# Kernel optimization log

Measured on AMD Instinct MI355X. Metric: run time of the kernel, lower is better.

The kernel has to match this reference:

```python
import jax, jax.numpy as jnp
import numpy as np
from jax import lax

KSIZE, STRIDE, RATE, SOFTMAX_SCALE = 3, 1, 2, 10.0


def extract_patches(x, k, stride):
    # x: [B,C,H,W] -> [B,C,k,k,oh,ow]; torch-style zero 'same' padding
    B, C, H, W = x.shape
    oh, ow = -(-H // stride), -(-W // stride)
    ph = max(0, (oh - 1) * stride + k - H)
    pw = max(0, (ow - 1) * stride + k - W)
    x = jnp.pad(x, ((0, 0), (0, 0), (ph // 2, ph - ph // 2), (pw // 2, pw - pw // 2)))
    cols = [x[:, :, i:i + (oh - 1) * stride + 1:stride, j:j + (ow - 1) * stride + 1:stride]
            for i in range(k) for j in range(k)]
    return jnp.stack(cols, axis=2).reshape(B, C, k, k, oh, ow)


def setup_inputs():
    key = jax.random.key(0)
    kf, kb = jax.random.split(key)
    f = jax.random.normal(kf, (2, 128, 128, 128), dtype=jnp.float32)
    b = jax.random.normal(kb, (2, 128, 128, 128), dtype=jnp.float32)
    mask = jnp.zeros((2, 1, 512, 512), dtype=jnp.float32)
    mask = mask.at[:, :, 128:384, 128:384].set(1.0)  # central hole: bg patches unavailable
    return {"f": f, "b": b, "mask": mask}


def reference(f, b, mask):
    B, C, H, W = b.shape
    kernel = 2 * RATE
    # raw background patches used for reconstruction (stride = rate*stride)
    raw = extract_patches(b, kernel, RATE * STRIDE)            # [B,C,4,4,Hb,Wb]
    Hb, Wb = raw.shape[-2:]
    L = Hb * Wb
    raw_w = raw.transpose(0, 4, 5, 1, 2, 3).reshape(B, L, C, kernel, kernel)
    # nearest 1/rate downsample (integer rate -> strided slice)
    fs = f[:, :, ::RATE, ::RATE]
    bs = b[:, :, ::RATE, ::RATE]
    Hf, Wf = fs.shape[-2:]
    # matching patches from downsampled background, L2-normalized per patch
    wp = extract_patches(bs, KSIZE, STRIDE)                    # [B,C,3,3,Hb,Wb]
    w = wp.transpose(0, 4, 5, 1, 2, 3).reshape(B, L, C, KSIZE, KSIZE)
    norm = jnp.sqrt(jnp.sum(w * w, axis=(2, 3, 4), keepdims=True))
    w_normed = w / jnp.maximum(norm, 1e-4)
    # mask -> per-patch validity (original uses batch element 0 only)
    ms = mask[:, :, ::4 * RATE, ::4 * RATE]                    # [B,1,Hb,Wb]
    mp = extract_patches(ms, KSIZE, STRIDE)[0]                 # [1,3,3,Hb,Wb]
    mm = (jnp.mean(mp, axis=(0, 1, 2)).reshape(-1) == 0.0).astype(f.dtype)
    mm = mm.reshape(1, L, 1, 1)
    # similarity scores: per-image conv2d of fg with bg patches == patch einsum
    fp = extract_patches(fs, KSIZE, STRIDE)                    # [B,C,3,3,Hf,Wf]
    yi = jnp.einsum('bcpqhw,blcpq->blhw', fp, w_normed)        # [B,L,Hf,Wf]
    yi = yi * mm
    yi = jax.nn.softmax(yi * SOFTMAX_SCALE, axis=1)
    yi = yi * mm
    # argmax offsets relative to reference coordinates (int_bs == int_fs here)
    off = jnp.argmax(yi, axis=1)                               # [B,Hf,Wf]
    h_ref = jnp.arange(Hf)[None, :, None]
    w_ref = jnp.arange(Wf)[None, None, :]
    offsets = jnp.stack([off // Wf - h_ref, off % Wf - w_ref], axis=1)  # [B,2,Hf,Wf]
    # reconstruction: conv_transpose2d(yi, raw_wi, stride=rate, padding=1) / 4
    w_ct = jnp.flip(raw_w.transpose(0, 2, 1, 3, 4), axis=(-2, -1))      # [B,C,L,4,4]
    pad = kernel - 1 - 1  # transpose-conv padding=1 -> conv pad k-1-1
    def ct(a, wk):
        return lax.conv_general_dilated(a[None], wk, (1, 1),
                                        ((pad, pad), (pad, pad)),
                                        lhs_dilation=(RATE, RATE),
                                        dimension_numbers=('NCHW', 'OIHW', 'NCHW'))[0]
    y = jax.vmap(ct)(yi, w_ct) / 4.0                           # [B,C,H,W]
    return y, offsets
```

## Files before the change

### kernel.cpp

```cpp
#include <hip/hip_runtime.h>
#include <hip/hip_bf16.h>
#include <cstdint>

#define B_  2
#define C_  128
#define HH  128
#define WW  128
#define L_  4096
#define K1  1152
#define M2  2048
#define NPAD 3072
#define NCAND 16
#define MARGIN 0.15f
#define PCUT 5e-4f
#define MAXC 512

typedef __attribute__((ext_vector_type(8))) short bf16x8s;
typedef __attribute__((ext_vector_type(4))) float f32x4;
typedef __attribute__((ext_vector_type(2))) float f32x2;
using bf16 = __hip_bfloat16;

__device__ inline float bf16bits2f(unsigned short s) {
  uint32_t u = ((uint32_t)s) << 16;
  return __builtin_bit_cast(float, u);
}
__device__ inline unsigned short f2bf16bits(float x) {
  uint32_t u = __builtin_bit_cast(uint32_t, x);
  u += 0x7fffu + ((u >> 16) & 1u);
  return (unsigned short)(u >> 16);
}

__device__ inline uint8_t fp8_encode(float v) {
  uint32_t s = (__builtin_bit_cast(uint32_t, v) >> 24) & 0x80u;
  float av = fabsf(v);
  uint32_t byte;
  if (av >= 0.015625f) {
    uint32_t bits = __builtin_bit_cast(uint32_t, av);
    uint32_t mant = bits & 0x7fffffu;
    uint32_t E = bits >> 23;
    uint32_t m3 = (mant + 0x7ffffu + ((mant >> 20) & 1u)) >> 20;
    if (m3 == 8u) { m3 = 0u; E++; }
    int e8 = (int)E - 120;
    if (e8 > 15) { e8 = 15; m3 = 6; }
    byte = ((uint32_t)e8 << 3) | m3;
  } else {
    byte = (uint32_t)(av * 512.f + 0.5f);
  }
  return (uint8_t)(s | byte);
}

#if __has_builtin(__builtin_amdgcn_cvt_pk_f32_fp8)
#define FP8PK(d, hi) __builtin_amdgcn_cvt_pk_f32_fp8((d), (hi))
#else
__device__ inline f32x2 FP8PK(uint32_t d, bool hi) {
  uint32_t b0 = hi ? ((d >> 16) & 0xffu) : (d & 0xffu);
  uint32_t b1 = hi ? (d >> 24) : ((d >> 8) & 0xffu);
  f32x2 r;
  r.x = __builtin_bit_cast(float, ((b0 & 0x80u) << 24) | ((b0 & 0x7fu) << 20)) * 0x1p120f;
  r.y = __builtin_bit_cast(float, ((b1 & 0x80u) << 24) | ((b1 & 0x7fu) << 20)) * 0x1p120f;
  return r;
}
#endif

__device__ inline void gload_lds16(const void* g, void* l) {
  auto gp = reinterpret_cast<const __attribute__((address_space(1))) uint32_t*>(
      reinterpret_cast<uintptr_t>(g));
  auto lp = reinterpret_cast<__attribute__((address_space(3))) uint32_t*>(
      reinterpret_cast<uintptr_t>(l));
  __builtin_amdgcn_global_load_lds(gp, lp, 16, 0, 0);
}

__global__ void compute_mm_k(const float* __restrict__ mask, float* __restrict__ mm) {
  int l = blockIdx.x * 256 + threadIdx.x;
  if (l >= L_) return;
  int i = l >> 6, j = l & 63;
  float s = 0.f;
  for (int p = -1; p <= 1; ++p)
    for (int q = -1; q <= 1; ++q) {
      int y = i + p, x = j + q;
      if ((unsigned)y < 64u && (unsigned)x < 64u)
        s += mask[(size_t)(8 * y) * 512 + 8 * x];
    }
  mm[l] = (s == 0.f) ? 1.f : 0.f;
}

__global__ __launch_bounds__(256) void compact_k(const float* __restrict__ mm,
                                                 int* __restrict__ vlist,
                                                 int* __restrict__ vmap,
                                                 int* __restrict__ meta) {
  __shared__ int wpart[4];
  int t = threadIdx.x;
  int lane = t & 63, wid = t >> 6;
  int loc[16];
  int cnt = 0;
#pragma unroll
  for (int s = 0; s < 16; ++s) {
    int l = t * 16 + s;
    loc[s] = cnt;
    cnt += (mm[l] != 0.f) ? 1 : 0;
  }
  int pre = cnt;
#pragma unroll
  for (int o = 1; o < 64; o <<= 1) {
    int u = __shfl_up(pre, o);
    if (lane >= o) pre += u;
  }
  if (lane == 63) wpart[wid] = pre;
  int excl = pre - cnt;
  __syncthreads();
  int base = 0;
  for (int w = 0; w < wid; ++w) base += wpart[w];
  int mybase = base + excl;
#pragma unroll
  for (int s = 0; s < 16; ++s) {
    int l = t * 16 + s;
    if (mm[l] != 0.f) {
      int pos = mybase + loc[s];
      vlist[pos] = l;
      vmap[l] = pos;
    }
  }
  if (t == 0) {
    int total = wpart[0] + wpart[1] + wpart[2] + wpart[3];
    meta[0] = total;
    meta[1] = L_ - total;
  }
}

__global__ __launch_bounds__(256) void prep_u_k(const float* __restrict__ bsrc,
                                                const float* __restrict__ mm,
                                                const int* __restrict__ vmap,
                                                bf16* __restrict__ Ucomp,
                                                float* __restrict__ U32) {
  __shared__ float red[4];
  int l = blockIdx.x;
  int bi = blockIdx.y;
  if (mm[l] == 0.f) return;
  int pos = vmap[l];
  int i = l >> 6, j = l & 63;
  int t = threadIdx.x;
  float vals[5];
  float ss = 0.f;
#pragma unroll
  for (int s = 0; s < 5; ++s) {
    int k = t + s * 256;
    float v = 0.f;
    if (k < K1) {
      int c = k / 9, r = k - c * 9;
      int p = r / 3, q = r - p * 3;
      int y = i + p - 1, x = j + q - 1;
      if ((unsigned)y < 64u && (unsigned)x < 64u)
        v = bsrc[(((size_t)bi * C_ + c) * HH + 2 * y) * WW + 2 * x];
    }
    vals[s] = v;
    ss += v * v;
  }
#pragma unroll
  for (int o = 32; o; o >>= 1) ss += __shfl_xor(ss, o);
  if ((t & 63) == 0) red[t >> 6] = ss;
  __syncthreads();
  float tot = red[0] + red[1] + red[2] + red[3];
  float den = fmaxf(sqrtf(tot), 1e-4f);
  float inv = 1.f / den;
  size_t cbase = ((size_t)bi * NPAD + pos) * K1;
  size_t obase = ((size_t)bi * L_ + l) * K1;
#pragma unroll
  for (int s = 0; s < 5; ++s) {
    int k = t + s * 256;
    if (k < K1) {
      float u = vals[s] * inv;
      Ucomp[cbase + k] = __float2bfloat16(u);
      U32[obase + k] = u;
    }
  }
}

__global__ __launch_bounds__(256) void prep_fp_k(const float* __restrict__ f,
                                                 bf16* __restrict__ FP,
                                                 float* __restrict__ FP32) {
  int idx = blockIdx.x * 256 + threadIdx.x;
  int bi = blockIdx.y;
  if (idx >= L_ * K1) return;
  int hw = idx / K1, k = idx - hw * K1;
  int h = hw >> 6, w = hw & 63;
  int c = k / 9, r = k - c * 9;
  int p = r / 3, q = r - p * 3;
  int y = h + p - 1, x = w + q - 1;
  float v = 0.f;
  if ((unsigned)y < 64u && (unsigned)x < 64u)
    v = f[(((size_t)bi * C_ + c) * HH + 2 * y) * WW + 2 * x];
  size_t o = (size_t)bi * L_ * K1 + idx;
  FP[o] = __float2bfloat16(v);
  FP32[o] = v;
}

__global__ void prep_bmatT_k(const float* __restrict__ bsrc, uint8_t* __restrict__ BmT8) {
  int idx = blockIdx.x * 256 + threadIdx.x;
  int bi = blockIdx.y;
  if (idx >= M2 * L_) return;
  int l = idx >> 11, m = idx & 2047;
  int c = m >> 4, p = (m >> 2) & 3, q = m & 3;
  int i = l >> 6, j = l & 63;
  int y = 2 * i + p - 1, x = 2 * j + q - 1;
  float v = 0.f;
  if ((unsigned)y < 128u && (unsigned)x < 128u)
    v = bsrc[(((size_t)bi * C_ + c) * HH + y) * WW + x];
  BmT8[(size_t)bi * M2 * L_ + idx] = fp8_encode(v);
}

__global__ __launch_bounds__(256) void gemm_bt(const bf16* __restrict__ A,
                                               const bf16* __restrict__ Bbase,
                                               bf16* __restrict__ C,
                                               int N, int K) {
  __shared__ __align__(16) bf16 sA[2][128][32];
  __shared__ __align__(16) bf16 sB[2][128][32];
  const int tid = threadIdx.x;
  const int lane = tid & 63;
  const int wid = tid >> 6;
  const int bm = blockIdx.x * 128;
  const int bn = blockIdx.y * 128;
  const bf16* B = Bbase + (size_t)(bm >> 12) * NPAD * K1;
  const int wm = (wid >> 1) * 64;
  const int wn = (wid & 1) * 64;
  const int lrow = lane & 15;
  const int lko = (lane >> 4) * 8;

  f32x4 acc[4][4];
#pragma unroll
  for (int i = 0; i < 4; ++i)
#pragma unroll
    for (int j = 0; j < 4; ++j) acc[i][j] = (f32x4){0.f, 0.f, 0.f, 0.f};

  const int nt = K >> 5;
  const int s0 = tid, s1 = tid + 256;
  const int ar0 = s0 >> 2, ac0 = (s0 & 3) * 8;
  const int ar1 = s1 >> 2, ac1 = (s1 & 3) * 8;

  auto STAGE = [&](int bufi, int t) {
    const int k0 = t * 32;
    gload_lds16(A + (size_t)(bm + ar0) * K + k0 + ac0, &sA[bufi][ar0][ac0]);
    gload_lds16(A + (size_t)(bm + ar1) * K + k0 + ac1, &sA[bufi][ar1][ac1]);
    gload_lds16(B + (size_t)(bn + ar0) * K + k0 + ac0, &sB[bufi][ar0][ac0]);
    gload_lds16(B + (size_t)(bn + ar1) * K + k0 + ac1, &sB[bufi][ar1][ac1]);
  };

  STAGE(0, 0);
  __syncthreads();
  int buf = 0;
  for (int t = 0; t < nt; ++t) {
    if (t + 1 < nt) STAGE(buf ^ 1, t + 1);
    bf16x8s af[4], bfr[4];
#pragma unroll
    for (int fm = 0; fm < 4; ++fm)
      af[fm] = *(const bf16x8s*)&sA[buf][wm + fm * 16 + lrow][lko];
#pragma unroll
    for (int fn = 0; fn < 4; ++fn)
      bfr[fn] = *(const bf16x8s*)&sB[buf][wn + fn * 16 + lrow][lko];
#pragma unroll
    for (int fm = 0; fm < 4; ++fm)
#pragma unroll
      for (int fn = 0; fn < 4; ++fn)
        acc[fm][fn] = __builtin_amdgcn_mfma_f32_16x16x32_bf16(af[fm], bfr[fn], acc[fm][fn], 0, 0, 0);
    __syncthreads();
    buf ^= 1;
  }

  const int crow = (lane >> 4) * 4;
  const int ccol = lane & 15;
#pragma unroll
  for (int fm = 0; fm < 4; ++fm)
#pragma unroll
    for (int fn = 0; fn < 4; ++fn) {
      int r0 = bm + wm + fm * 16 + crow;
      int c0 = bn + wn + fn * 16 + ccol;
#pragma unroll
      for (int r = 0; r < 4; ++r)
        C[(size_t)(r0 + r) * N + c0] = __float2bfloat16(acc[fm][fn][r]);
    }
}

__global__ __launch_bounds__(256) void softmax_spmv_k(const bf16* __restrict__ Sb,
                                                      const int* __restrict__ vlist,
                                                      const int* __restrict__ meta,
                                                      const uint8_t* __restrict__ BmT8b,
                                                      unsigned short* __restrict__ Ztb,
                                                      int* __restrict__ candb,
                                                      int* __restrict__ candcntb) {
  __shared__ float rmax[4];
  __shared__ float rsum[4];
  __shared__ int scnt, mcnt;
  __shared__ int slist[MAXC];
  __shared__ float splist[MAXC];
  __shared__ int mlist[NCAND];
  const int row = blockIdx.x;
  const int bi = blockIdx.y;
  const int t = threadIdx.x;
  const int vcnt = meta[0];
  const int nmask = meta[1];
  const uint8_t* BmT8 = BmT8b + (size_t)bi * M2 * L_;
  if (t == 0) { scnt = 0; mcnt = 0; }
  const bool has = (t < NPAD / 16);
  const int c0 = t * 16;
  float xs[16];
#pragma unroll
  for (int s = 0; s < 16; ++s) xs[s] = -1e30f;
  if (has) {
    const bf16* srow = Sb + ((size_t)bi * L_ + row) * NPAD;
    bf16x8s sv0 = *(const bf16x8s*)&srow[c0];
    bf16x8s sv1 = *(const bf16x8s*)&srow[c0 + 8];
#pragma unroll
    for (int s = 0; s < 8; ++s) {
      xs[s] = bf16bits2f((unsigned short)sv0[s]);
      xs[s + 8] = bf16bits2f((unsigned short)sv1[s]);
    }
  }
  float vmax = -1e30f;
#pragma unroll
  for (int s = 0; s < 16; ++s)
    if (has && c0 + s < vcnt) vmax = fmaxf(vmax, xs[s]);
#pragma unroll
  for (int o = 32; o; o >>= 1) vmax = fmaxf(vmax, __shfl_xor(vmax, o));
  if ((t & 63) == 0) rmax[t >> 6] = vmax;
  __syncthreads();
  vmax = fmaxf(fmaxf(rmax[0], rmax[1]), fmaxf(rmax[2], rmax[3]));
  float gmax = (nmask > 0) ? fmaxf(vmax, 0.f) : vmax;
  float zs = 0.f;
#pragma unroll
  for (int s = 0; s < 16; ++s)
    if (has && c0 + s < vcnt) zs += __expf(10.f * (xs[s] - gmax));
#pragma unroll
  for (int o = 32; o; o >>= 1) zs += __shfl_xor(zs, o);
  if ((t & 63) == 0) rsum[t >> 6] = zs;
  __syncthreads();
  zs = rsum[0] + rsum[1] + rsum[2] + rsum[3] + (float)nmask * __expf(-10.f * gmax);
  float invZ = 1.f / zs;
  float cutx = gmax + __logf(PCUT * zs) * 0.1f;
  if (has) {
#pragma unroll
    for (int s = 0; s < 16; ++s) {
      int c = c0 + s;
      if (c < vcnt) {
        if (xs[s] >= cutx) {
          int pos = atomicAdd(&scnt, 1);
          if (pos < MAXC) {
            slist[pos] = vlist[c];
            splist[pos] = __expf(10.f * (xs[s] - gmax)) * invZ;
          }
        }
        if (xs[s] >= vmax - MARGIN) {
          int pos = atomicAdd(&mcnt, 1);
          if (pos < NCAND) mlist[pos] = vlist[c];
        }
      }
    }
  }
  __syncthreads();
  int nc = min(scnt, MAXC);
  float acc[8] = {0.f, 0.f, 0.f, 0.f, 0.f, 0.f, 0.f, 0.f};
#pragma unroll 4
  for (int ci = 0; ci < nc; ++ci) {
    int l = slist[ci];
    float p = splist[ci];
    const uint32_t* bp = (const uint32_t*)(BmT8 + (size_t)l * M2) + t * 2;
    uint32_t d0 = bp[0], d1 = bp[1];
    f32x2 w0 = FP8PK(d0, false);
    f32x2 w1 = FP8PK(d0, true);
    f32x2 w2 = FP8PK(d1, false);
    f32x2 w3 = FP8PK(d1, true);
    acc[0] += p * w0.x; acc[1] += p * w0.y;
    acc[2] += p * w1.x; acc[3] += p * w1.y;
    acc[4] += p * w2.x; acc[5] += p * w2.y;
    acc[6] += p * w3.x; acc[7] += p * w3.y;
  }
  bf16x8s zv;
#pragma unroll
  for (int j = 0; j < 8; ++j) zv[j] = (short)f2bf16bits(acc[j]);
  *(bf16x8s*)&Ztb[((size_t)bi * L_ + row) * M2 + t * 8] = zv;
  if (t == 0) candcntb[bi * L_ + row] = min(mcnt, NCAND);
  if (t < NCAND && t < mcnt) candb[(bi * L_ + row) * NCAND + t] = mlist[t];
}

__global__ __launch_bounds__(256) void transpose_k(const unsigned short* __restrict__ inb,
                                                   unsigned short* __restrict__ outb) {
  __shared__ ushort2 tile[32][33];
  int bi = blockIdx.z;
  const unsigned short* in = inb + (size_t)bi * L_ * M2;
  unsigned short* out = outb + (size_t)bi * M2 * L_;
  int bm2 = blockIdx.x * 32;
  int bh = blockIdx.y * 32;
  int tx = threadIdx.x & 31;
  int ty = threadIdx.x >> 5;
  const ushort2* in2 = (const ushort2*)in;
#pragma unroll
  for (int r = 0; r < 32; r += 8)
    tile[ty + r][tx] = in2[(size_t)(bh + ty + r) * (M2 / 2) + bm2 + tx];
  __syncthreads();
#pragma unroll
  for (int r = 0; r < 32; r += 8) {
    ushort2 v = tile[tx][ty + r];
    int mp = bm2 + ty + r;
    out[(size_t)(2 * mp) * L_ + bh + tx] = v.x;
    out[(size_t)(2 * mp + 1) * L_ + bh + tx] = v.y;
  }
}

__global__ __launch_bounds__(256) void rescore_k(const float* __restrict__ FP32b,
                                                 const float* __restrict__ U32b,
                                                 const int* __restrict__ candb,
                                                 const int* __restrict__ candcntb,
                                                 float* __restrict__ offout) {
  __shared__ float red[4];
  const int row = blockIdx.x;
  const int bi = blockIdx.y;
  const int t = threadIdx.x;
  const int h = row >> 6, w = row & 63;
  const float* FP32 = FP32b + (size_t)bi * L_ * K1;
  const float* U32 = U32b + (size_t)bi * L_ * K1;
  const int* cand = candb + (size_t)(bi * L_ + row) * NCAND;
  int cnt = candcntb[bi * L_ + row];
  int bestl;
  if (cnt <= 1) {
    bestl = cand[0];
  } else {
    float fv[5];
#pragma unroll
    for (int s = 0; s < 5; ++s) {
      int k = t + s * 256;
      fv[s] = (k < K1) ? FP32[(size_t)row * K1 + k] : 0.f;
    }
    float bestv = -1e30f;
    bestl = 0x7fffffff;
    for (int ci = 0; ci < cnt; ++ci) {
      int l = cand[ci];
      const float* urow = U32 + (size_t)l * K1;
      float dot = 0.f;
#pragma unroll
      for (int s = 0; s < 5; ++s) {
        int k = t + s * 256;
        if (k < K1) dot += fv[s] * urow[k];
      }
#pragma unroll
      for (int o = 32; o; o >>= 1) dot += __shfl_xor(dot, o);
      if ((t & 63) == 0) red[t >> 6] = dot;
      __syncthreads();
      dot = red[0] + red[1] + red[2] + red[3];
      if (dot > bestv || (dot == bestv && l < bestl)) { bestv = dot; bestl = l; }
      __syncthreads();
    }
  }
  if (t == 0) {
    int istar = bestl >> 6, jstar = bestl & 63;
    offout[(size_t)bi * 8192 + row] = (float)(istar - h);
    offout[(size_t)bi * 8192 + L_ + row] = (float)(jstar - w);
  }
}

__global__ void gather_k(const unsigned short* __restrict__ Z2b, float* __restrict__ yout) {
  int u = blockIdx.x, c = blockIdx.y, bi = blockIdx.z;
  int t = threadIdx.x;
  const unsigned short* Z2 = Z2b + (size_t)bi * M2 * L_;
  int h0 = (u + 1) >> 1, p0 = (u + 1) & 1;
  int h1 = h0 - 1, p1 = p0 + 2;
  float a0 = 0.f, a1 = 0.f;
#pragma unroll
  for (int e = 0; e < 2; ++e) {
    int h = e ? h1 : h0;
    int p = e ? p1 : p0;
    if ((unsigned)h < 64u) {
      const unsigned short* zb = Z2 + (size_t)(c * 16 + p * 4) * L_ + h * 64;
      a0 += bf16bits2f(zb[1 * L_ + t]);
      if (t >= 1) a0 += bf16bits2f(zb[3 * L_ + (t - 1)]);
      if (t < 63) a1 += bf16bits2f(zb[0 * L_ + (t + 1)]);
      a1 += bf16bits2f(zb[2 * L_ + t]);
    }
  }
  size_t ybase = (((size_t)bi * C_ + c) * HH + u) * WW;
  yout[ybase + 2 * t] = a0 * 0.25f;
  yout[ybase + 2 * t + 1] = a1 * 0.25f;
}

extern "C" void kernel_launch(void* const* d_in, const int* in_sizes, int n_in,
                              void* d_out, int out_size, void* d_ws, size_t ws_size,
                              hipStream_t stream) {
  const float* f = (const float*)d_in[0];
  const float* b = (const float*)d_in[1];
  const float* mask = (const float*)d_in[2];
  float* out = (float*)d_out;
  char* ws = (char*)d_ws;

  size_t off = 0;
  float* mm = (float*)(ws + off);          off += 16384;
  int* vlist = (int*)(ws + off);           off += 16384;
  int* vmap = (int*)(ws + off);            off += 16384;
  int* meta = (int*)(ws + off);            off += 16384;
  int* cand = (int*)(ws + off);            off += (size_t)B_ * L_ * NCAND * 4;
  int* candcnt = (int*)(ws + off);         off += 65536;
  bf16* Ucomp = (bf16*)(ws + off);         off += (size_t)B_ * NPAD * K1 * 2;
  bf16* FP = (bf16*)(ws + off);            off += (size_t)B_ * L_ * K1 * 2;
  float* U32 = (float*)(ws + off);         off += (size_t)B_ * L_ * K1 * 4;
  float* FP32 = (float*)(ws + off);        off += (size_t)B_ * L_ * K1 * 4;
  uint8_t* BmT8 = (uint8_t*)(ws + off);    off += (size_t)B_ * M2 * L_;
  bf16* S = (bf16*)(ws + off);             off += (size_t)B_ * L_ * NPAD * 2;
  unsigned short* Zt = (unsigned short*)(ws + off); off += (size_t)B_ * M2 * L_ * 2;
  unsigned short* Z2 = (unsigned short*)(ws + off); off += (size_t)B_ * M2 * L_ * 2;
  float* yout = out;
  float* offout = out + (size_t)B_ * C_ * HH * WW;

  compute_mm_k<<<16, 256, 0, stream>>>(mask, mm);
  compact_k<<<1, 256, 0, stream>>>(mm, vlist, vmap, meta);
  prep_u_k<<<dim3(L_, B_), 256, 0, stream>>>(b, mm, vmap, Ucomp, U32);
  prep_fp_k<<<dim3((L_ * K1 + 255) / 256, B_), 256, 0, stream>>>(f, FP, FP32);
  prep_bmatT_k<<<dim3((M2 * L_ + 255) / 256, B_), 256, 0, stream>>>(b, BmT8);
  gemm_bt<<<dim3(B_ * L_ / 128, NPAD / 128), 256, 0, stream>>>(FP, Ucomp, S, NPAD, K1);
  softmax_spmv_k<<<dim3(L_, B_), 256, 0, stream>>>(S, vlist, meta, BmT8, Zt, cand, candcnt);
  rescore_k<<<dim3(L_, B_), 256, 0, stream>>>(FP32, U32, cand, candcnt, offout);
  transpose_k<<<dim3(M2 / 64, L_ / 32, B_), 256, 0, stream>>>(Zt, Z2);
  gather_k<<<dim3(128, 128, B_), 64, 0, stream>>>(Z2, yout);
}
```

Measured before the change: 256.9 us.

## Enlarge GEMM tiles to 256x256 with triple-buffered LDS pipeline

The similarity GEMM moves from 128x128 tiles with 256 threads and double buffering to 256x256 tiles with 512 threads, 8x4 MFMA fragments per wave, and a three-slot LDS ring. Loads are issued two stages ahead, with manual vmcnt waits and s_barrier in place of __syncthreads. MFMA sections are wrapped in s_setprio. The aim is more data reuse per LDS byte and better hiding of global-load latency, at the cost of more registers and fewer blocks (32x12 grid), which could reduce occupancy and load balance.

```diff
diff --git a/kernel.cpp b/kernel.cpp
--- a/kernel.cpp
+++ b/kernel.cpp
@@ -14,6 +14,11 @@
 #define MARGIN 0.15f
 #define PCUT 5e-4f
 #define MAXC 512
+
+#define BMG 256
+#define BNG 256
+#define BKG 32
+#define NBUF 3
 
 typedef __attribute__((ext_vector_type(8))) short bf16x8s;
 typedef __attribute__((ext_vector_type(4))) float f32x4;
@@ -208,67 +213,84 @@
   BmT8[(size_t)bi * M2 * L_ + idx] = fp8_encode(v);
 }
 
-__global__ __launch_bounds__(256) void gemm_bt(const bf16* __restrict__ A,
-                                               const bf16* __restrict__ Bbase,
-                                               bf16* __restrict__ C,
-                                               int N, int K) {
-  __shared__ __align__(16) bf16 sA[2][128][32];
-  __shared__ __align__(16) bf16 sB[2][128][32];
+__global__ __launch_bounds__(512, 2) void gemm_bt(const bf16* __restrict__ A,
+                                                  const bf16* __restrict__ Bbase,
+                                                  bf16* __restrict__ C,
+                                                  int N, int K) {
+  extern __shared__ char smem[];
+  bf16 (*sA)[BMG][BKG] = (bf16(*)[BMG][BKG])smem;
+  bf16 (*sB)[BNG][BKG] = (bf16(*)[BNG][BKG])(smem + (size_t)NBUF * BMG * BKG * 2);
   const int tid = threadIdx.x;
   const int lane = tid & 63;
   const int wid = tid >> 6;
-  const int bm = blockIdx.x * 128;
-  const int bn = blockIdx.y * 128;
+  const int bm = blockIdx.x * BMG;
+  const int bn = blockIdx.y * BNG;
   const bf16* B = Bbase + (size_t)(bm >> 12) * NPAD * K1;
-  const int wm = (wid >> 1) * 64;
-  const int wn = (wid & 1) * 64;
+  const int wm = (wid >> 2) * 128;
+  const int wn = (wid & 3) * 64;
   const int lrow = lane & 15;
   const int lko = (lane >> 4) * 8;
 
-  f32x4 acc[4][4];
-#pragma unroll
-  for (int i = 0; i < 4; ++i)
+  f32x4 acc[8][4];
+#pragma unroll
+  for (int i = 0; i < 8; ++i)
 #pragma unroll
     for (int j = 0; j < 4; ++j) acc[i][j] = (f32x4){0.f, 0.f, 0.f, 0.f};
 
   const int nt = K >> 5;
-  const int s0 = tid, s1 = tid + 256;
-  const int ar0 = s0 >> 2, ac0 = (s0 & 3) * 8;
-  const int ar1 = s1 >> 2, ac1 = (s1 & 3) * 8;
-
-  auto STAGE = [&](int bufi, int t) {
-    const int k0 = t * 32;
-    gload_lds16(A + (size_t)(bm + ar0) * K + k0 + ac0, &sA[bufi][ar0][ac0]);
-    gload_lds16(A + (size_t)(bm + ar1) * K + k0 + ac1, &sA[bufi][ar1][ac1]);
-    gload_lds16(B + (size_t)(bn + ar0) * K + k0 + ac0, &sB[bufi][ar0][ac0]);
-    gload_lds16(B + (size_t)(bn + ar1) * K + k0 + ac1, &sB[bufi][ar1][ac1]);
+  const int srow = tid >> 2;
+  const int scol = (tid & 3) * 8;
+
+  auto STAGE = [&](int slot, int t) {
+    const int k0 = t * BKG;
+    gload_lds16(A + (size_t)(bm + srow) * K + k0 + scol,        &sA[slot][srow][scol]);
+    gload_lds16(A + (size_t)(bm + 128 + srow) * K + k0 + scol,  &sA[slot][128 + srow][scol]);
+    gload_lds16(B + (size_t)(bn + srow) * K + k0 + scol,        &sB[slot][srow][scol]);
+    gload_lds16(B + (size_t)(bn + 128 + srow) * K + k0 + scol,  &sB[slot][128 + srow][scol]);
   };
 
   STAGE(0, 0);
-  __syncthreads();
-  int buf = 0;
+  STAGE(1, 1);
+  asm volatile("s_waitcnt vmcnt(4)" ::: "memory");
+  asm volatile("s_barrier" ::: "memory");
+
+  int slot = 0;
   for (int t = 0; t < nt; ++t) {
-    if (t + 1 < nt) STAGE(buf ^ 1, t + 1);
-    bf16x8s af[4], bfr[4];
-#pragma unroll
-    for (int fm = 0; fm < 4; ++fm)
-      af[fm] = *(const bf16x8s*)&sA[buf][wm + fm * 16 + lrow][lko];
+    int s2 = slot + 2; if (s2 >= NBUF) s2 -= NBUF;
+    if (t + 2 < nt) STAGE(s2, t + 2);
+
+    bf16x8s bfr[4];
 #pragma unroll
     for (int fn = 0; fn < 4; ++fn)
-      bfr[fn] = *(const bf16x8s*)&sB[buf][wn + fn * 16 + lrow][lko];
-#pragma unroll
-    for (int fm = 0; fm < 4; ++fm)
-#pragma unroll
-      for (int fn = 0; fn < 4; ++fn)
-        acc[fm][fn] = __builtin_amdgcn_mfma_f32_16x16x32_bf16(af[fm], bfr[fn], acc[fm][fn], 0, 0, 0);
-    __syncthreads();
-    buf ^= 1;
+      bfr[fn] = *(const bf16x8s*)&sB[slot][wn + fn * 16 + lrow][lko];
+#pragma unroll
+    for (int half = 0; half < 2; ++half) {
+      bf16x8s af[4];
+#pragma unroll
+      for (int fm = 0; fm < 4; ++fm)
+        af[fm] = *(const bf16x8s*)&sA[slot][wm + (half * 4 + fm) * 16 + lrow][lko];
+      __builtin_amdgcn_s_setprio(1);
+#pragma unroll
+      for (int fm = 0; fm < 4; ++fm)
+#pragma unroll
+        for (int fn = 0; fn < 4; ++fn)
+          acc[half * 4 + fm][fn] =
+              __builtin_amdgcn_mfma_f32_16x16x32_bf16(af[fm], bfr[fn], acc[half * 4 + fm][fn], 0, 0, 0);
+      __builtin_amdgcn_s_setprio(0);
+    }
+
+    if (t + 1 < nt) {
+      if (t + 2 < nt) asm volatile("s_waitcnt vmcnt(4)" ::: "memory");
+      else            asm volatile("s_waitcnt vmcnt(0)" ::: "memory");
+      asm volatile("s_barrier" ::: "memory");
+    }
+    slot = (slot + 1 == NBUF) ? 0 : slot + 1;
   }
 
   const int crow = (lane >> 4) * 4;
   const int ccol = lane & 15;
 #pragma unroll
-  for (int fm = 0; fm < 4; ++fm)
+  for (int fm = 0; fm < 8; ++fm)
 #pragma unroll
     for (int fn = 0; fn < 4; ++fn) {
       int r0 = bm + wm + fm * 16 + crow;
@@ -511,7 +533,8 @@
   prep_u_k<<<dim3(L_, B_), 256, 0, stream>>>(b, mm, vmap, Ucomp, U32);
   prep_fp_k<<<dim3((L_ * K1 + 255) / 256, B_), 256, 0, stream>>>(f, FP, FP32);
   prep_bmatT_k<<<dim3((M2 * L_ + 255) / 256, B_), 256, 0, stream>>>(b, BmT8);
-  gemm_bt<<<dim3(B_ * L_ / 128, NPAD / 128), 256, 0, stream>>>(FP, Ucomp, S, NPAD, K1);
+  gemm_bt<<<dim3(B_ * L_ / BMG, NPAD / BNG), 512,
+            (size_t)NBUF * (BMG + BNG) * BKG * 2, stream>>>(FP, Ucomp, S, NPAD, K1);
   softmax_spmv_k<<<dim3(L_, B_), 256, 0, stream>>>(S, vlist, meta, BmT8, Zt, cand, candcnt);
   rescore_k<<<dim3(L_, B_), 256, 0, stream>>>(FP32, U32, cand, candcnt, offout);
   transpose_k<<<dim3(M2 / 64, L_ / 32, B_), 256, 0, stream>>>(Zt, Z2);
```

New measurement: 262.7 us. +2.3%, slower.

## Triple-buffer GEMM LDS staging with split-phase MFMA and priority hints

Applied to the files above, without the earlier changes.

Moves the bf16 GEMM from a double-buffered to a triple-buffered LDS pipeline that prefetches two K-tiles ahead. Each iteration is split into two MFMA phases, with the A and B loads for a future tile interleaved between them. Explicit vmcnt waits, raw s_barriers and s_setprio are used to keep the matrix units busy while global-to-LDS copies are in flight. LDS use grows by half, which may reduce occupancy, and the extra barriers plus the hand-written waitcnt logic add synchronisation and correctness risk.

```diff
diff --git a/kernel.cpp b/kernel.cpp
--- a/kernel.cpp
+++ b/kernel.cpp
@@ -212,8 +212,8 @@
                                                const bf16* __restrict__ Bbase,
                                                bf16* __restrict__ C,
                                                int N, int K) {
-  __shared__ __align__(16) bf16 sA[2][128][32];
-  __shared__ __align__(16) bf16 sB[2][128][32];
+  __shared__ __align__(16) bf16 sA[3][128][32];
+  __shared__ __align__(16) bf16 sB[3][128][32];
   const int tid = threadIdx.x;
   const int lane = tid & 63;
   const int wid = tid >> 6;
@@ -236,33 +236,58 @@
   const int ar0 = s0 >> 2, ac0 = (s0 & 3) * 8;
   const int ar1 = s1 >> 2, ac1 = (s1 & 3) * 8;
 
-  auto STAGE = [&](int bufi, int t) {
+  auto STAGE_A = [&](int sl, int t) {
     const int k0 = t * 32;
-    gload_lds16(A + (size_t)(bm + ar0) * K + k0 + ac0, &sA[bufi][ar0][ac0]);
-    gload_lds16(A + (size_t)(bm + ar1) * K + k0 + ac1, &sA[bufi][ar1][ac1]);
-    gload_lds16(B + (size_t)(bn + ar0) * K + k0 + ac0, &sB[bufi][ar0][ac0]);
-    gload_lds16(B + (size_t)(bn + ar1) * K + k0 + ac1, &sB[bufi][ar1][ac1]);
+    gload_lds16(A + (size_t)(bm + ar0) * K + k0 + ac0, &sA[sl][ar0][ac0]);
+    gload_lds16(A + (size_t)(bm + ar1) * K + k0 + ac1, &sA[sl][ar1][ac1]);
   };
-
-  STAGE(0, 0);
-  __syncthreads();
-  int buf = 0;
+  auto STAGE_B = [&](int sl, int t) {
+    const int k0 = t * 32;
+    gload_lds16(B + (size_t)(bn + ar0) * K + k0 + ac0, &sB[sl][ar0][ac0]);
+    gload_lds16(B + (size_t)(bn + ar1) * K + k0 + ac1, &sB[sl][ar1][ac1]);
+  };
+
+  STAGE_A(0, 0); STAGE_B(0, 0);
+  STAGE_A(1, 1); STAGE_B(1, 1);
+  asm volatile("s_waitcnt vmcnt(4)" ::: "memory");
+  __builtin_amdgcn_s_barrier();
+
+  int slot = 0;
   for (int t = 0; t < nt; ++t) {
-    if (t + 1 < nt) STAGE(buf ^ 1, t + 1);
+    int s2 = slot + 2; if (s2 >= 3) s2 -= 3;
     bf16x8s af[4], bfr[4];
 #pragma unroll
     for (int fm = 0; fm < 4; ++fm)
-      af[fm] = *(const bf16x8s*)&sA[buf][wm + fm * 16 + lrow][lko];
-#pragma unroll
-    for (int fn = 0; fn < 4; ++fn)
-      bfr[fn] = *(const bf16x8s*)&sB[buf][wn + fn * 16 + lrow][lko];
+      af[fm] = *(const bf16x8s*)&sA[slot][wm + fm * 16 + lrow][lko];
+    bfr[0] = *(const bf16x8s*)&sB[slot][wn + lrow][lko];
+    bfr[1] = *(const bf16x8s*)&sB[slot][wn + 16 + lrow][lko];
+    if (t + 2 < nt) STAGE_A(s2, t + 2);
+    __builtin_amdgcn_s_barrier();
+    __builtin_amdgcn_s_setprio(1);
 #pragma unroll
     for (int fm = 0; fm < 4; ++fm)
 #pragma unroll
-      for (int fn = 0; fn < 4; ++fn)
+      for (int fn = 0; fn < 2; ++fn)
         acc[fm][fn] = __builtin_amdgcn_mfma_f32_16x16x32_bf16(af[fm], bfr[fn], acc[fm][fn], 0, 0, 0);
-    __syncthreads();
-    buf ^= 1;
+    __builtin_amdgcn_s_setprio(0);
+    __builtin_amdgcn_s_barrier();
+    bfr[2] = *(const bf16x8s*)&sB[slot][wn + 32 + lrow][lko];
+    bfr[3] = *(const bf16x8s*)&sB[slot][wn + 48 + lrow][lko];
+    if (t + 2 < nt) STAGE_B(s2, t + 2);
+    __builtin_amdgcn_s_barrier();
+    __builtin_amdgcn_s_setprio(1);
+#pragma unroll
+    for (int fm = 0; fm < 4; ++fm)
+#pragma unroll
+      for (int fn = 2; fn < 4; ++fn)
+        acc[fm][fn] = __builtin_amdgcn_mfma_f32_16x16x32_bf16(af[fm], bfr[fn], acc[fm][fn], 0, 0, 0);
+    __builtin_amdgcn_s_setprio(0);
+    if (t + 1 < nt) {
+      if (t + 2 < nt) asm volatile("s_waitcnt vmcnt(4)" ::: "memory");
+      else            asm volatile("s_waitcnt vmcnt(0)" ::: "memory");
+    }
+    __builtin_amdgcn_s_barrier();
+    slot = (slot + 1 == 3) ? 0 : slot + 1;
   }
 
   const int crow = (lane >> 4) * 4;
```

Result: no change. 260.1 us (+1.2%).
